# Performance work log

Hardware: AMD Instinct MI355X
Metric: run time of the kernel (lower is better)

Reference implementation:

```python
import jax, jax.numpy as jnp
import numpy as np
import math

N, D, H, KV, DH, E, F_, CH = 2048, 1024, 16, 4, 64, 8, 2048, 64
VOCAB = 32000
EPS = 1e-6
THETA = 10000.0
DT = 0.1
BASE_SCALE = 10.0


def rmsnorm(x, w):
    var = jnp.mean(jnp.square(x), axis=-1, keepdims=True)
    return x * jax.lax.rsqrt(var + EPS) * w


def rope_tables(positions):
    inv_freq = THETA ** (-jnp.arange(0, DH, 2, dtype=jnp.float32) / DH)  # [DH/2]
    ang = positions.astype(jnp.float32)[:, None] * inv_freq              # [N, DH/2]
    return jnp.cos(ang), jnp.sin(ang)


def apply_rotary(x, cos, sin):
    # x: [N, heads, DH]; NeoX half-split rotation
    x1, x2 = jnp.split(x, 2, axis=-1)
    c, s = cos[:, None, :], sin[:, None, :]
    return jnp.concatenate([x1 * c - x2 * s, x2 * c + x1 * s], axis=-1)


def setup_inputs() -> dict:
    key = jax.random.key(0)
    ks = jax.random.split(key, 20)
    nrm = lambda k, shp, std: (jax.random.normal(k, shp) * std).astype(jnp.float32)
    inp = {
        'hidden': jax.random.normal(ks[0], (N, D), jnp.float32),
        'positions': jnp.arange(N, dtype=jnp.int32),
        'velocity': jax.random.normal(ks[1], (N, D), jnp.float32) * 0.1,
        'token_ids': jax.random.randint(ks[2], (N,), 0, VOCAB),
        'mu_prev': jax.random.normal(ks[3], (N, D), jnp.float32) * 0.1,
        'ln1_w': jnp.ones((D,), jnp.float32),
        'ln2_w': jnp.ones((D,), jnp.float32),
        'wq': nrm(ks[4], (D, H * DH), 0.02),
        'wk': nrm(ks[5], (D, KV * DH), 0.02),
        'wv': nrm(ks[6], (D, KV * DH), 0.02),
        'wo': nrm(ks[7], (H * DH, D), 0.02),
        'w_mu_q': nrm(ks[8], (D, H * DH), 0.01),
        'w_mu_k': nrm(ks[9], (D, KV * DH), 0.01),
        'w_mu_v': nrm(ks[10], (D, KV * DH), 0.01),
        'qnorm_w': jnp.ones((DH,), jnp.float32),
        'knorm_w': jnp.ones((DH,), jnp.float32),
        'dyn_mu': jnp.zeros((D,), jnp.float32),
        'dyn_mu_proj_w': nrm(ks[11], (D, D), 0.01),
        'ctrl_in_w': nrm(ks[12], (2 * D, CH), 0.02),
        'ctrl_in_b': jnp.zeros((CH,), jnp.float32),
        'ctrl_out_w': nrm(ks[13], (CH, 3 * D), 0.01),
        'ctrl_out_b': jnp.concatenate([jnp.full((D,), 2.2), jnp.full((D,), -2.2), jnp.zeros((D,))]).astype(jnp.float32),
        'mu_router_w': nrm(ks[14], (D, E), 0.01),
        'w_gate': nrm(ks[15], (E, D, F_), 0.02),
        'w_up': nrm(ks[16], (E, D, F_), 0.02),
        'w_down': nrm(ks[17], (E, F_, D), 0.02),
    }
    return inp


def reference(hidden, positions, velocity, token_ids, mu_prev,
              ln1_w, ln2_w, wq, wk, wv, wo, w_mu_q, w_mu_k, w_mu_v,
              qnorm_w, knorm_w, dyn_mu, dyn_mu_proj_w,
              ctrl_in_w, ctrl_in_b, ctrl_out_w, ctrl_out_b,
              mu_router_w, w_gate, w_up, w_down):
    residual = hidden
    h = rmsnorm(hidden, ln1_w)
    # --- mu-guided GQA attention ---
    q = (h @ wq + mu_prev @ w_mu_q).reshape(N, H, DH)
    k = (h @ wk + mu_prev @ w_mu_k).reshape(N, KV, DH)
    v = (h @ wv + mu_prev @ w_mu_v).reshape(N, KV, DH)
    q = rmsnorm(q, qnorm_w)
    k = rmsnorm(k, knorm_w)
    cos, sin = rope_tables(positions)
    q = apply_rotary(q, cos, sin)
    k = apply_rotary(k, cos, sin)
    groups = H // KV
    k = jnp.repeat(k, groups, axis=1)  # [N, H, DH]
    v = jnp.repeat(v, groups, axis=1)
    scale = 1.0 / math.sqrt(DH)
    scores = jnp.einsum('nhd,mhd->hnm', q, k) * scale
    attn = jax.nn.softmax(scores, axis=-1)
    o = jnp.einsum('hnm,mhd->nhd', attn, v).reshape(N, H * DH) @ wo
    # --- INL dynamics (PID) ---
    hv = jnp.concatenate([o, velocity], axis=-1)
    ctrl = jax.nn.silu(hv @ ctrl_in_w + ctrl_in_b)
    co = ctrl @ ctrl_out_w + ctrl_out_b
    alpha_raw, beta_raw, gate_raw = co[:, :D], co[:, D:2 * D], co[:, 2 * D:]
    alpha = jax.nn.sigmoid(alpha_raw)
    beta = jnp.minimum(jax.nn.softplus(beta_raw), 2.0)
    gate = jax.nn.sigmoid(gate_raw)
    mu_cur = dyn_mu + o @ dyn_mu_proj_w
    err = o - mu_cur
    v_next = jnp.clip(alpha * velocity - beta * err, -10.0, 10.0)
    h_next = o + DT * gate * v_next
    hidden = residual + h_next
    # --- mu-guided token-routed MoE MLP ---
    residual2 = hidden
    x = rmsnorm(hidden, ln2_w)
    base_ids = (token_ids % E).astype(jnp.int32)
    mu_logits = mu_cur @ mu_router_w                        # [N, E]
    combined = jax.nn.one_hot(base_ids, E) * BASE_SCALE + mu_logits
    expert_ids = jnp.argmax(combined, axis=-1)              # [N]
    g = jnp.einsum('nd,edf->enf', x, w_gate)                # [E, N, F]
    u = jnp.einsum('nd,edf->enf', x, w_up)
    mid = jax.nn.silu(g) * u
    y_all = jnp.einsum('enf,efd->end', mid, w_down)         # [E, N, D]
    sel = jax.nn.one_hot(expert_ids, E)                     # [N, E]
    y = jnp.einsum('ne,end->nd', sel, y_all)
    hidden = residual2 + y
    return (hidden, v_next, mu_cur)
```

## Files before the change

### kernel.cpp

```cpp
#include <hip/hip_runtime.h>
#include <hip/hip_bf16.h>
#include <math.h>

typedef __hip_bfloat16 bf16;
typedef __attribute__((ext_vector_type(8))) short short8;
typedef __attribute__((ext_vector_type(4))) short short4v;
typedef __attribute__((ext_vector_type(4))) float floatx4;

#define N_TOK 2048
#define DM    1024
#define NH    16
#define NKV   4
#define DH    64
#define NE    8
#define FF    2048
#define CH    64
#define QSCL  0.18033688011112042f

__device__ __forceinline__ float b2f(bf16 x) { return __bfloat162float(x); }
__device__ __forceinline__ bf16  f2b(float x) { return __float2bfloat16(x); }
__device__ __forceinline__ short f2s(float x) { bf16 t = __float2bfloat16(x); return *(short*)&t; }

#define MFMA16(a, b, c) __builtin_amdgcn_mfma_f32_16x16x32_bf16(a, b, c, 0, 0, 0)

#define GLL16(g, l) __builtin_amdgcn_global_load_lds( \
    (const __attribute__((address_space(1))) void*)(g), \
    (__attribute__((address_space(3))) void*)(l), 16, 0, 0)

__device__ __forceinline__ float blockReduceSum256(float v) {
    __shared__ float tmp[4];
    #pragma unroll
    for (int m = 1; m < 64; m <<= 1) v += __shfl_xor(v, m, 64);
    if ((threadIdx.x & 63) == 0) tmp[threadIdx.x >> 6] = v;
    __syncthreads();
    float r = tmp[0] + tmp[1] + tmp[2] + tmp[3];
    __syncthreads();
    return r;
}

struct TEnt {
    const float* src; bf16* dst;
    long sstride, dstride;
    int sN, ldk, tN, tilesPer, start;
};
struct TTab { TEnt t[13]; };

template <int TK>
__global__ __launch_bounds__(256) void k_transpose_all(TTab tab, int base,
                                                       int* counts, int* fill) {
    if (base == 0 && blockIdx.x == 0 && threadIdx.x < NE) {
        counts[threadIdx.x] = 0;
        fill[threadIdx.x] = 0;
    }
    int b = blockIdx.x + base;
    int wi = 0;
    #pragma unroll
    for (int i = 1; i < 13; i++) if (b >= tab.t[i].start) wi = i;
    const TEnt& w = tab.t[wi];
    int local = b - w.start;
    int e = local / w.tilesPer; local -= e * w.tilesPer;
    int kt = local / w.tN, nt = local - kt * w.tN;
    const float* s = w.src + (long)e * w.sstride + (long)(kt * TK) * w.sN + nt * 64;
    bf16* d = w.dst + (long)e * w.dstride + (long)(nt * 64) * w.ldk + kt * TK;

    __shared__ short t16[64 * TK];
    int tid = threadIdx.x;
    int c4 = (tid & 15) * 4;

    #pragma unroll
    for (int j = 0; j < (TK / 8 + 15) / 16; j++) {
        int kk8 = 8 * ((tid >> 4) + 16 * j);
        if (kk8 < TK) {
            float4 rr[8];
            #pragma unroll
            for (int t = 0; t < 8; t++)
                rr[t] = *(const float4*)(s + (long)(kk8 + t) * w.sN + c4);
            #pragma unroll
            for (int q = 0; q < 4; q++) {
                int n = c4 + q;
                int ks = kk8 ^ ((n & 7) << 3);
                short8 o;
                #pragma unroll
                for (int t = 0; t < 8; t++) o[t] = f2s(((const float*)&rr[t])[q]);
                *(short8*)&t16[n * TK + ks] = o;
            }
        }
    }
    __syncthreads();
    const int cpr = TK / 8;
    #pragma unroll
    for (int rnd = 0; rnd < TK / 32; rnd++) {
        int id = tid + rnd * 256;
        int n = id / cpr;
        int kc = (id % cpr) * 8;
        int ks = kc ^ ((n & 7) << 3);
        short8 o = *(const short8*)&t16[n * TK + ks];
        *(short8*)(d + (long)n * w.ldk + kc) = o;
    }
}

__global__ __launch_bounds__(256) void k_prep(
    const float* __restrict__ hidden, const float* __restrict__ ln1_w,
    const float* __restrict__ mu_prev, const float* __restrict__ velocity,
    bf16* __restrict__ catA, bf16* __restrict__ ctrlA)
{
    int n = blockIdx.x, tid = threadIdx.x;
    float ss = 0.f, vals[4];
    #pragma unroll
    for (int i = 0; i < 4; i++) {
        int c = tid + i * 256;
        vals[i] = hidden[(long)n * DM + c];
        ss += vals[i] * vals[i];
        catA[(long)n * 2048 + 1024 + c] = f2b(mu_prev[(long)n * DM + c]);
        ctrlA[(long)n * 2048 + 1024 + c] = f2b(velocity[(long)n * DM + c]);
    }
    float tot = blockReduceSum256(ss);
    float r = rsqrtf(tot / (float)DM + 1e-6f);
    #pragma unroll
    for (int i = 0; i < 4; i++) {
        int c = tid + i * 256;
        catA[(long)n * 2048 + c] = f2b(vals[i] * r * ln1_w[c]);
    }
}

#define GEMM_WRITE  1
#define GEMM_BIAS   2
#define GEMM_WRITEB 4

__global__ __launch_bounds__(256) void k_gemm(
    const bf16* __restrict__ A, int lda,
    const bf16* __restrict__ Bt, int ldb, long strideBe,
    float* __restrict__ C, int ldc,
    const float* __restrict__ bias,
    bf16* __restrict__ Cb, int ldcb,
    int K, int flags,
    int nsplit, long strideKc,
    const int* __restrict__ grp_cnt)
{
    __shared__ __align__(16) short As[128 * 32];
    __shared__ __align__(16) short Bs[128 * 32];
    int tid = threadIdx.x;
    int e = blockIdx.z, kc = 0;
    if (nsplit > 1) { e = blockIdx.z / nsplit; kc = blockIdx.z % nsplit; }
    int rowBase, rowsValid;
    const bf16* Bp = Bt;
    if (grp_cnt) {
        int r0 = 0;
        #pragma unroll
        for (int i = 0; i < NE; i++) r0 += (i < e) ? grp_cnt[i] : 0;
        int r1 = r0 + grp_cnt[e];
        int rt = blockIdx.y * 128;
        rowsValid = (r1 - r0) - rt;
        if (rowsValid <= 0) return;
        if (rowsValid > 128) rowsValid = 128;
        rowBase = r0 + rt;
        Bp = Bt + (long)e * strideBe;
    } else {
        rowBase = blockIdx.y * 128;
        rowsValid = 128;
    }
    int n0 = blockIdx.x * 128;
    int Kc = K / nsplit;
    int kbeg = kc * Kc, kend = kbeg + Kc;

    floatx4 acc[4][4];
    #pragma unroll
    for (int i = 0; i < 4; i++)
        #pragma unroll
        for (int j = 0; j < 4; j++) acc[i][j] = (floatx4){0.f, 0.f, 0.f, 0.f};

    int wave = tid >> 6, lane = tid & 63;
    int wm = (wave >> 1) * 64, wn = (wave & 1) * 64;
    int lrow = lane & 15, quad = lane >> 4;

    int c0 = wave * 2;
    int srow0 = c0 * 16 + (lane >> 2);
    int srow1 = (c0 + 1) * 16 + (lane >> 2);
    int skoff = (lane & 3) * 8;
    short* ldsA0 = As + c0 * 512;
    short* ldsA1 = As + (c0 + 1) * 512;
    short* ldsB0 = Bs + c0 * 512;
    short* ldsB1 = Bs + (c0 + 1) * 512;

    for (int k0 = kbeg; k0 < kend; k0 += 32) {
        if (srow0 < rowsValid) GLL16(A + (long)(rowBase + srow0) * lda + k0 + skoff, ldsA0);
        if (srow1 < rowsValid) GLL16(A + (long)(rowBase + srow1) * lda + k0 + skoff, ldsA1);
        GLL16(Bp + (long)(n0 + srow0) * ldb + k0 + skoff, ldsB0);
        GLL16(Bp + (long)(n0 + srow1) * ldb + k0 + skoff, ldsB1);
        __syncthreads();
        short8 af[4], bfr[4];
        #pragma unroll
        for (int mi = 0; mi < 4; mi++)
            af[mi] = *(const short8*)(&As[(wm + mi * 16 + lrow) * 32 + quad * 8]);
        #pragma unroll
        for (int ni = 0; ni < 4; ni++)
            bfr[ni] = *(const short8*)(&Bs[(wn + ni * 16 + lrow) * 32 + quad * 8]);
        #pragma unroll
        for (int mi = 0; mi < 4; mi++)
            #pragma unroll
            for (int ni = 0; ni < 4; ni++)
                acc[mi][ni] = MFMA16(af[mi], bfr[ni], acc[mi][ni]);
        __syncthreads();
    }

    #pragma unroll
    for (int mi = 0; mi < 4; mi++) {
        #pragma unroll
        for (int ni = 0; ni < 4; ni++) {
            #pragma unroll
            for (int r = 0; r < 4; r++) {
                int rl = wm + mi * 16 + quad * 4 + r;
                if (rl >= rowsValid) continue;
                int grow = rowBase + rl;
                int gcol = n0 + wn + ni * 16 + lrow;
                float v = acc[mi][ni][r];
                if (nsplit > 1) {
                    C[kc * strideKc + (long)grow * ldc + gcol] = v;
                    continue;
                }
                if (flags & GEMM_BIAS) v += bias[gcol];
                if (flags & GEMM_WRITE) C[(long)grow * ldc + gcol] = v;
                if (flags & GEMM_WRITEB) Cb[(long)grow * ldcb + gcol] = f2b(v);
            }
        }
    }
}

__global__ __launch_bounds__(256) void k_gemm_f32b(
    const bf16* __restrict__ A, int lda,
    const float* __restrict__ Bf0, const float* __restrict__ Bf1,
    int ldbn, long strideBfe, int nbf0,
    float* __restrict__ C, int ldc,
    bf16* __restrict__ Cb, int ldcb,
    int K, int flags,
    int nsplit, long strideKc,
    const int* __restrict__ grp_cnt)
{
    __shared__ __align__(16) short As[128 * 32];
    __shared__ __align__(16) float Braw[32 * 128];
    __shared__ __align__(16) short Bs2[128 * 40];
    int tid = threadIdx.x;
    int e = blockIdx.z, kc = 0;
    if (nsplit > 1) { e = blockIdx.z / nsplit; kc = blockIdx.z % nsplit; }
    int r0 = 0;
    #pragma unroll
    for (int i = 0; i < NE; i++) r0 += (i < e) ? grp_cnt[i] : 0;
    int r1 = r0 + grp_cnt[e];
    int rt = blockIdx.y * 128;
    int rowsValid = (r1 - r0) - rt;
    if (rowsValid <= 0) return;
    if (rowsValid > 128) rowsValid = 128;
    int rowBase = r0 + rt;

    int n0 = blockIdx.x * 128;
    const float* Bsrc;
    int nb;
    if (n0 < nbf0) { Bsrc = Bf0; nb = n0; }
    else           { Bsrc = Bf1; nb = n0 - nbf0; }
    Bsrc += (long)e * strideBfe;

    int Kc = K / nsplit;
    int kbeg = kc * Kc, kend = kbeg + Kc;

    floatx4 acc[4][4];
    #pragma unroll
    for (int i = 0; i < 4; i++)
        #pragma unroll
        for (int j = 0; j < 4; j++) acc[i][j] = (floatx4){0.f, 0.f, 0.f, 0.f};

    int wave = tid >> 6, lane = tid & 63;
    int wm = (wave >> 1) * 64, wn = (wave & 1) * 64;
    int lrow = lane & 15, quad = lane >> 4;

    int c0 = wave * 2;
    int srow0 = c0 * 16 + (lane >> 2);
    int srow1 = (c0 + 1) * 16 + (lane >> 2);
    int skoff = (lane & 3) * 8;
    short* ldsA0 = As + c0 * 512;
    short* ldsA1 = As + (c0 + 1) * 512;

    int kB = wave * 2 + (lane >> 5);
    int ncB = (lane & 31) * 4;

    for (int k0 = kbeg; k0 < kend; k0 += 32) {
        if (srow0 < rowsValid) GLL16(A + (long)(rowBase + srow0) * lda + k0 + skoff, ldsA0);
        if (srow1 < rowsValid) GLL16(A + (long)(rowBase + srow1) * lda + k0 + skoff, ldsA1);
        #pragma unroll
        for (int r = 0; r < 4; r++)
            GLL16(Bsrc + (long)(k0 + r * 8 + kB) * ldbn + nb + ncB,
                  Braw + r * 1024 + wave * 256);
        __syncthreads();

        #pragma unroll
        for (int r2 = 0; r2 < 4; r2++) {
            int id = r2 * 256 + tid;
            int n = id & 127, kb = id >> 7;
            float f0 = Braw[(kb * 4 + 0) * 128 + n];
            float f1 = Braw[(kb * 4 + 1) * 128 + n];
            float f2 = Braw[(kb * 4 + 2) * 128 + n];
            float f3 = Braw[(kb * 4 + 3) * 128 + n];
            short4v o;
            o[0] = f2s(f0); o[1] = f2s(f1); o[2] = f2s(f2); o[3] = f2s(f3);
            *(short4v*)&Bs2[n * 40 + kb * 4] = o;
        }
        short8 af[4];
        #pragma unroll
        for (int mi = 0; mi < 4; mi++)
            af[mi] = *(const short8*)(&As[(wm + mi * 16 + lrow) * 32 + quad * 8]);
        __syncthreads();

        short8 bfr[4];
        #pragma unroll
        for (int ni = 0; ni < 4; ni++)
            bfr[ni] = *(const short8*)(&Bs2[(wn + ni * 16 + lrow) * 40 + quad * 8]);
        #pragma unroll
        for (int mi = 0; mi < 4; mi++)
            #pragma unroll
            for (int ni = 0; ni < 4; ni++)
                acc[mi][ni] = MFMA16(af[mi], bfr[ni], acc[mi][ni]);
    }
    __syncthreads();

    #pragma unroll
    for (int mi = 0; mi < 4; mi++) {
        #pragma unroll
        for (int ni = 0; ni < 4; ni++) {
            #pragma unroll
            for (int r = 0; r < 4; r++) {
                int rl = wm + mi * 16 + quad * 4 + r;
                if (rl >= rowsValid) continue;
                int grow = rowBase + rl;
                int gcol = n0 + wn + ni * 16 + lrow;
                float v = acc[mi][ni][r];
                if (nsplit > 1) {
                    C[kc * strideKc + (long)grow * ldc + gcol] = v;
                } else if (flags & GEMM_WRITEB) {
                    Cb[(long)grow * ldcb + gcol] = f2b(v);
                }
            }
        }
    }
}

__global__ __launch_bounds__(256) void k_red_wo(const float* __restrict__ p,
                                                float* __restrict__ o_f,
                                                bf16* __restrict__ ctrlA) {
    int n = blockIdx.x, tid = threadIdx.x;
    #pragma unroll
    for (int i = 0; i < 4; i++) {
        int c = tid + i * 256;
        float v = p[(long)n * DM + c] + p[(long)N_TOK * DM + (long)n * DM + c];
        o_f[(long)n * DM + c] = v;
        ctrlA[(long)n * 2048 + c] = f2b(v);
    }
}

__global__ __launch_bounds__(256) void k_red_down(const float* __restrict__ p,
                                                  const int* __restrict__ perm,
                                                  float* __restrict__ out0) {
    int r = blockIdx.x, tid = threadIdx.x;
    int tok = perm[r];
    #pragma unroll
    for (int i = 0; i < 4; i++) {
        int c = tid + i * 256;
        long idx = (long)r * DM + c;
        float v = p[idx] + p[(long)N_TOK * DM + idx] +
                  p[(long)2 * N_TOK * DM + idx] + p[(long)3 * N_TOK * DM + idx];
        out0[(long)tok * DM + c] += v;
    }
}

__global__ __launch_bounds__(256) void k_ctrl_gemm(
    const bf16* __restrict__ A,
    const bf16* __restrict__ Bt,
    float* __restrict__ part)
{
    __shared__ __align__(16) short As[128 * 32];
    __shared__ __align__(16) short Bs[64 * 32];
    int tid = threadIdx.x;
    int rowBase = blockIdx.x * 128;
    int kbeg = blockIdx.y * 256;
    int wave = tid >> 6, lane = tid & 63;
    int wm = wave * 32, lrow = lane & 15, quad = lane >> 4;
    int srow = lane >> 2, skoff = (lane & 3) * 8;

    floatx4 acc[2][4];
    #pragma unroll
    for (int i = 0; i < 2; i++)
        #pragma unroll
        for (int j = 0; j < 4; j++) acc[i][j] = (floatx4){0.f, 0.f, 0.f, 0.f};

    short* ldsA0 = As + (wave * 2) * 512;
    short* ldsA1 = As + (wave * 2 + 1) * 512;
    short* ldsB  = Bs + wave * 512;

    for (int k0 = kbeg; k0 < kbeg + 256; k0 += 32) {
        GLL16(A + (long)(rowBase + wave * 32 + srow) * 2048 + k0 + skoff, ldsA0);
        GLL16(A + (long)(rowBase + wave * 32 + 16 + srow) * 2048 + k0 + skoff, ldsA1);
        GLL16(Bt + (long)(wave * 16 + srow) * 2048 + k0 + skoff, ldsB);
        __syncthreads();
        short8 af[2], bfr[4];
        af[0] = *(const short8*)(&As[(wm + lrow) * 32 + quad * 8]);
        af[1] = *(const short8*)(&As[(wm + 16 + lrow) * 32 + quad * 8]);
        #pragma unroll
        for (int ni = 0; ni < 4; ni++)
            bfr[ni] = *(const short8*)(&Bs[(ni * 16 + lrow) * 32 + quad * 8]);
        #pragma unroll
        for (int mi = 0; mi < 2; mi++)
            #pragma unroll
            for (int ni = 0; ni < 4; ni++)
                acc[mi][ni] = MFMA16(af[mi], bfr[ni], acc[mi][ni]);
        __syncthreads();
    }
    #pragma unroll
    for (int mi = 0; mi < 2; mi++)
        #pragma unroll
        for (int ni = 0; ni < 4; ni++)
            #pragma unroll
            for (int r = 0; r < 4; r++) {
                int grow = rowBase + wm + mi * 16 + quad * 4 + r;
                part[((long)blockIdx.y * N_TOK + grow) * 64 + ni * 16 + lrow] = acc[mi][ni][r];
            }
}

__global__ __launch_bounds__(256) void k_silu_ctrl(const float* __restrict__ part,
                                                   const float* __restrict__ b,
                                                   bf16* __restrict__ out) {
    int i4 = (blockIdx.x * 256 + threadIdx.x) * 4;
    float4 a = *(const float4*)(b + (i4 & 63));
    #pragma unroll
    for (int kc = 0; kc < 8; kc++) {
        float4 p = *(const float4*)(part + (long)kc * (N_TOK * 64) + i4);
        a.x += p.x; a.y += p.y; a.z += p.z; a.w += p.w;
    }
    short4v o;
    o[0] = f2s(a.x / (1.f + __expf(-a.x)));
    o[1] = f2s(a.y / (1.f + __expf(-a.y)));
    o[2] = f2s(a.z / (1.f + __expf(-a.z)));
    o[3] = f2s(a.w / (1.f + __expf(-a.w)));
    *(short4v*)(out + i4) = o;
}

__global__ __launch_bounds__(256) void k_qkv_post(
    const float* __restrict__ qkvp, const int* __restrict__ positions,
    const float* __restrict__ qnw, const float* __restrict__ knw,
    bf16* __restrict__ q, bf16* __restrict__ k, bf16* __restrict__ v)
{
    int n = blockIdx.x;
    int wave = threadIdx.x >> 6, lane = threadIdx.x & 63;
    float pos = (float)positions[n];
    int i = lane & 31;
    float invf = exp2f(-(float)(2 * i) * (13.287712379549449f / 64.f));
    float ang = pos * invf;
    float c = cosf(ang), s = sinf(ang);

    #pragma unroll
    for (int si = 0; si < 6; si++) {
        int slot = wave + si * 4;
        long base = (long)n * 1536 +
                    (slot < 16 ? slot * 64
                               : (slot < 20 ? 1024 + (slot - 16) * 64
                                            : 1280 + (slot - 20) * 64));
        float val = qkvp[base + lane] + qkvp[(long)N_TOK * 1536 + base + lane];
        if (slot < 20) {
            float ss = val * val;
            #pragma unroll
            for (int m = 1; m < 64; m <<= 1) ss += __shfl_xor(ss, m, 64);
            float r = rsqrtf(ss / 64.f + 1e-6f);
            float wn = (slot < 16 ? qnw[lane] : knw[lane]);
            float xn = val * r * wn;
            float partner = __shfl_xor(xn, 32, 64);
            float out = (lane < 32) ? (xn * c - partner * s) : (xn * c + partner * s);
            if (slot < 16) q[((long)n * NH + slot) * 64 + lane] = f2b(out * QSCL);
            else           k[((long)n * NKV + (slot - 16)) * 64 + lane] = f2b(out);
        } else {
            v[((long)n * NKV + (slot - 20)) * 64 + lane] = f2b(val);
        }
    }
}

__global__ __launch_bounds__(256) void k_vt(const bf16* __restrict__ v,
                                            bf16* __restrict__ vt) {
    __shared__ short tile[64][65];
    int kv = blockIdx.z, n0 = blockIdx.x * 64;
    int tid = threadIdx.x;
    int c = tid & 63, r4 = tid >> 6;
    const short* vs = (const short*)v;
    #pragma unroll
    for (int i = 0; i < 16; i++) {
        int r = i * 4 + r4;
        tile[r][c] = vs[(long)(n0 + r) * 256 + kv * 64 + c];
    }
    __syncthreads();
    #pragma unroll
    for (int i = 0; i < 16; i++) {
        int d = i * 4 + r4;
        ((short*)vt)[(long)(kv * 64 + d) * 2048 + n0 + c] = tile[c][d];
    }
}

__device__ __forceinline__ int lds_idx(int row, int col_sh) {
    int byteoff = col_sh * 2;
    byteoff ^= (row & 7) << 4;
    return row * 64 + (byteoff >> 1);
}

__global__ __launch_bounds__(256) void k_attn(
    const bf16* __restrict__ q, const bf16* __restrict__ k,
    const bf16* __restrict__ vt,
    float* __restrict__ opart, float2* __restrict__ ml)
{
    const int h = blockIdx.y;
    const int qbase = blockIdx.x * 64;
    const int z = blockIdx.z;
    const int kvh = h >> 2;
    __shared__ __align__(16) short Ks[64 * 64];
    __shared__ __align__(16) short Vt[64 * 64];
    __shared__ __align__(16) short Ps[64 * 64];
    int tid = threadIdx.x, wave = tid >> 6, lane = tid & 63;
    int lrow = lane & 15, quad = lane >> 4;

    const bf16* qp = q + ((long)(qbase + wave * 16 + lrow) * NH + h) * 64;
    short8 aq0 = *(const short8*)(qp + quad * 8);
    short8 aq1 = *(const short8*)(qp + 32 + quad * 8);

    short8 bones;
    #pragma unroll
    for (int j = 0; j < 8; j++) bones[j] = (short)0x3F80;

    const int lin0 = tid, lin1 = tid + 256;
    const int sr0 = lin0 >> 3, sc0 = (lin0 & 7) * 8;
    const int sr1 = lin1 >> 3, sc1 = (lin1 & 7) * 8;
    const int wi0 = lds_idx(sr0, sc0), wi1 = lds_idx(sr1, sc1);

    const int kt0 = z * (N_TOK / 4);
    const bf16* kg0 = k + ((long)(kt0 + sr0) * NKV + kvh) * 64 + sc0;
    const bf16* kg1 = k + ((long)(kt0 + sr1) * NKV + kvh) * 64 + sc1;
    const bf16* vg0 = vt + (long)(kvh * 64 + sr0) * 2048 + kt0 + sc0;
    const bf16* vg1 = vt + (long)(kvh * 64 + sr1) * 2048 + kt0 + sc1;

    *(short8*)&Ks[wi0] = *(const short8*)kg0;
    *(short8*)&Ks[wi1] = *(const short8*)kg1;
    *(short8*)&Vt[wi0] = *(const short8*)vg0;
    *(short8*)&Vt[wi1] = *(const short8*)vg1;

    float m_i[4];
    floatx4 lacc = (floatx4){0.f, 0.f, 0.f, 0.f};
    floatx4 oacc[4];
    #pragma unroll
    for (int r = 0; r < 4; r++) m_i[r] = -1e30f;
    #pragma unroll
    for (int di = 0; di < 4; di++) oacc[di] = (floatx4){0.f, 0.f, 0.f, 0.f};
    __syncthreads();

    const int NT = (N_TOK / 4) / 64;
    for (int t = 0; t < NT; t++) {
        bool pf = (t + 1 < NT);
        short8 nk0, nk1, nv0, nv1;
        if (pf) {
            long ko = (long)(t + 1) * (64 * NKV * 64);
            int  vo = (t + 1) * 64;
            nk0 = *(const short8*)(kg0 + ko);
            nk1 = *(const short8*)(kg1 + ko);
            nv0 = *(const short8*)(vg0 + vo);
            nv1 = *(const short8*)(vg1 + vo);
        }

        floatx4 sv[4];
        __builtin_amdgcn_s_setprio(1);
        #pragma unroll
        for (int kn = 0; kn < 4; kn++) {
            short8 b0 = *(const short8*)&Ks[lds_idx(kn * 16 + lrow, quad * 8)];
            short8 b1 = *(const short8*)&Ks[lds_idx(kn * 16 + lrow, 32 + quad * 8)];
            floatx4 tt = (floatx4){0.f, 0.f, 0.f, 0.f};
            tt = MFMA16(aq0, b0, tt);
            tt = MFMA16(aq1, b1, tt);
            sv[kn] = tt;
        }
        __builtin_amdgcn_s_setprio(0);

        float mx[4];
        #pragma unroll
        for (int r = 0; r < 4; r++) {
            float m0 = fmaxf(fmaxf(sv[0][r], sv[1][r]), fmaxf(sv[2][r], sv[3][r]));
            #pragma unroll
            for (int msk = 1; msk < 16; msk <<= 1) m0 = fmaxf(m0, __shfl_xor(m0, msk, 64));
            mx[r] = m0;
        }
        int ok = (mx[0] <= m_i[0] + 8.f) & (mx[1] <= m_i[1] + 8.f) &
                 (mx[2] <= m_i[2] + 8.f) & (mx[3] <= m_i[3] + 8.f);
        if (!__all(ok)) {
            #pragma unroll
            for (int r = 0; r < 4; r++) {
                float mn = fmaxf(m_i[r], mx[r]);
                float al = exp2f(m_i[r] - mn);
                m_i[r] = mn;
                lacc[r] *= al;
                #pragma unroll
                for (int di = 0; di < 4; di++) oacc[di][r] *= al;
            }
        }
        #pragma unroll
        for (int kn = 0; kn < 4; kn++)
            #pragma unroll
            for (int r = 0; r < 4; r++)
                sv[kn][r] = exp2f(sv[kn][r] - m_i[r]);

        #pragma unroll
        for (int kn = 0; kn < 4; kn++)
            #pragma unroll
            for (int r = 0; r < 4; r++)
                Ps[lds_idx(wave * 16 + quad * 4 + r, kn * 16 + lrow)] = f2s(sv[kn][r]);
        __syncthreads();

        short8 ap0 = *(const short8*)&Ps[lds_idx(wave * 16 + lrow, quad * 8)];
        short8 ap1 = *(const short8*)&Ps[lds_idx(wave * 16 + lrow, 32 + quad * 8)];
        __builtin_amdgcn_s_setprio(1);
        lacc = MFMA16(ap0, bones, lacc);
        lacc = MFMA16(ap1, bones, lacc);
        #pragma unroll
        for (int di = 0; di < 4; di++) {
            short8 bv0 = *(const short8*)&Vt[lds_idx(di * 16 + lrow, quad * 8)];
            short8 bv1 = *(const short8*)&Vt[lds_idx(di * 16 + lrow, 32 + quad * 8)];
            oacc[di] = MFMA16(ap0, bv0, oacc[di]);
            oacc[di] = MFMA16(ap1, bv1, oacc[di]);
        }
        __builtin_amdgcn_s_setprio(0);
        __syncthreads();

        if (pf) {
            *(short8*)&Ks[wi0] = nk0;
            *(short8*)&Ks[wi1] = nk1;
            *(short8*)&Vt[wi0] = nv0;
            *(short8*)&Vt[wi1] = nv1;
            __syncthreads();
        }
    }

    #pragma unroll
    for (int di = 0; di < 4; di++)
        #pragma unroll
        for (int r = 0; r < 4; r++) {
            int n = qbase + wave * 16 + quad * 4 + r;
            opart[((long)z * N_TOK + n) * DM + h * 64 + di * 16 + lrow] = oacc[di][r];
        }
    if (lrow == 0) {
        #pragma unroll
        for (int r = 0; r < 4; r++) {
            int n = qbase + wave * 16 + quad * 4 + r;
            ml[(long)(z * NH + h) * N_TOK + n] = make_float2(m_i[r], lacc[r]);
        }
    }
}

__global__ __launch_bounds__(256) void k_attn_merge(
    const float* __restrict__ opart, const float2* __restrict__ ml,
    bf16* __restrict__ attn_out)
{
    int n = blockIdx.x, tid = threadIdx.x;
    __shared__ float2 sml[4][NH];
    if (tid < 64) {
        int zz = tid >> 4, hh = tid & 15;
        sml[zz][hh] = ml[(long)(zz * NH + hh) * N_TOK + n];
    }
    __syncthreads();
    #pragma unroll
    for (int i = 0; i < 4; i++) {
        int c = tid + i * 256;
        int h = c >> 6;
        float M = fmaxf(fmaxf(sml[0][h].x, sml[1][h].x),
                        fmaxf(sml[2][h].x, sml[3][h].x));
        float num = 0.f, den = 0.f;
        #pragma unroll
        for (int zz = 0; zz < 4; zz++) {
            float w = exp2f(sml[zz][h].x - M);
            num += w * opart[((long)zz * N_TOK + n) * DM + c];
            den += w * sml[zz][h].y;
        }
        attn_out[(long)n * DM + c] = f2b(num / den);
    }
}

__global__ __launch_bounds__(256) void k_ode(
    const float* __restrict__ co, const float* __restrict__ o_f,
    const float* __restrict__ velocity, const float* __restrict__ mup,
    const float* __restrict__ dyn_mu, const float* __restrict__ hidden_in,
    const float* __restrict__ mu_router_w, const int* __restrict__ token_ids,
    const float* __restrict__ ln2_w,
    float* __restrict__ out0, float* __restrict__ out_vnext,
    float* __restrict__ out_mu, bf16* __restrict__ x_bf,
    int* __restrict__ expert_id, int* __restrict__ counts)
{
    int n = blockIdx.x, tid = threadIdx.x;
    __shared__ float mu_s[DM];
    __shared__ float red2[32][8];

    #pragma unroll
    for (int i = 0; i < 4; i++) {
        int c = tid + i * 256;
        mu_s[c] = mup[(long)n * DM + c] + mup[(long)N_TOK * DM + (long)n * DM + c]
                + dyn_mu[c];
    }
    __syncthreads();

    {
        int e = tid & 7, kc = tid >> 3;
        float a = 0.f;
        #pragma unroll
        for (int kk = 0; kk < 32; kk++) {
            int k = kc * 32 + kk;
            a += mu_s[k] * mu_router_w[k * NE + e];
        }
        red2[kc][e] = a;
    }
    __syncthreads();
    if (tid == 0) {
        int bid = token_ids[n] & (NE - 1);
        float best = -1e30f; int bi = 0;
        for (int e = 0; e < NE; e++) {
            float lg = (e == bid ? 10.f : 0.f);
            for (int j = 0; j < 32; j++) lg += red2[j][e];
            if (lg > best) { best = lg; bi = e; }
        }
        expert_id[n] = bi;
        atomicAdd(&counts[bi], 1);
    }

    float ssq = 0.f;
    float h1v[4];
    #pragma unroll
    for (int i = 0; i < 4; i++) {
        int c = tid + i * 256;
        float coa = co[(long)n * 3072 + c];
        float cob = co[(long)n * 3072 + DM + c];
        float cog = co[(long)n * 3072 + 2 * DM + c];
        float alpha = 1.f / (1.f + __expf(-coa));
        float sp = (cob > 20.f) ? cob : log1pf(__expf(cob));
        float beta = fminf(sp, 2.0f);
        float gate = 1.f / (1.f + __expf(-cog));
        float ov = o_f[(long)n * DM + c];
        float vv = velocity[(long)n * DM + c];
        float err = ov - mu_s[c];
        float vn = fminf(fmaxf(alpha * vv - beta * err, -10.f), 10.f);
        float hn = ov + 0.1f * gate * vn;
        float h1 = hidden_in[(long)n * DM + c] + hn;
        h1v[i] = h1;
        ssq += h1 * h1;
        out_vnext[(long)n * DM + c] = vn;
        out_mu[(long)n * DM + c] = mu_s[c];
        out0[(long)n * DM + c] = h1;
    }
    float tot = blockReduceSum256(ssq);
    float rstd = rsqrtf(tot / (float)DM + 1e-6f);
    #pragma unroll
    for (int i = 0; i < 4; i++) {
        int c = tid + i * 256;
        x_bf[(long)n * DM + c] = f2b(h1v[i] * rstd * ln2_w[c]);
    }
}

__global__ __launch_bounds__(256) void k_scatter_gather(
    const int* __restrict__ expert_id, const int* __restrict__ counts,
    int* __restrict__ fill, int* __restrict__ perm,
    const bf16* __restrict__ x, bf16* __restrict__ xg)
{
    int n = blockIdx.x * 4 + (threadIdx.x >> 6);
    int lane = threadIdx.x & 63;
    int e = expert_id[n];
    int p = 0;
    if (lane == 0) {
        int off = 0;
        #pragma unroll
        for (int i = 0; i < NE; i++) off += (i < e) ? counts[i] : 0;
        p = off + atomicAdd(&fill[e], 1);
        perm[p] = n;
    }
    p = __shfl(p, 0, 64);
    const int4* s = (const int4*)(x + (long)n * DM);
    int4* d = (int4*)(xg + (long)p * DM);
    d[lane] = s[lane];
    d[lane + 64] = s[lane + 64];
}

__global__ __launch_bounds__(256) void k_silumul(const bf16* __restrict__ gu,
                                                 bf16* __restrict__ mid) {
    long i = ((long)blockIdx.x * 256 + threadIdx.x) * 8;
    long r = i >> 11, c = i & 2047;
    short8 g8 = *(const short8*)(gu + r * 4096 + c);
    short8 u8 = *(const short8*)(gu + r * 4096 + 2048 + c);
    short8 o;
    #pragma unroll
    for (int j = 0; j < 8; j++) {
        short gs = g8[j], us = u8[j];
        float g = b2f(*(bf16*)&gs);
        float u = b2f(*(bf16*)&us);
        o[j] = f2s(g / (1.f + __expf(-g)) * u);
    }
    *(short8*)(mid + i) = o;
}

extern "C" void kernel_launch(void* const* d_in, const int* in_sizes, int n_in,
                              void* d_out, int out_size, void* d_ws, size_t ws_size,
                              hipStream_t stream) {
    (void)in_sizes; (void)n_in; (void)out_size; (void)ws_size;
    const float* hidden     = (const float*)d_in[0];
    const int*   positions  = (const int*)d_in[1];
    const float* velocity   = (const float*)d_in[2];
    const int*   token_ids  = (const int*)d_in[3];
    const float* mu_prev    = (const float*)d_in[4];
    const float* ln1_w      = (const float*)d_in[5];
    const float* ln2_w      = (const float*)d_in[6];
    const float* wq         = (const float*)d_in[7];
    const float* wk         = (const float*)d_in[8];
    const float* wv         = (const float*)d_in[9];
    const float* wo         = (const float*)d_in[10];
    const float* w_mu_q     = (const float*)d_in[11];
    const float* w_mu_k     = (const float*)d_in[12];
    const float* w_mu_v     = (const float*)d_in[13];
    const float* qnorm_w    = (const float*)d_in[14];
    const float* knorm_w    = (const float*)d_in[15];
    const float* dyn_mu     = (const float*)d_in[16];
    const float* dyn_proj   = (const float*)d_in[17];
    const float* ctrl_in_w  = (const float*)d_in[18];
    const float* ctrl_in_b  = (const float*)d_in[19];
    const float* ctrl_out_w = (const float*)d_in[20];
    const float* ctrl_out_b = (const float*)d_in[21];
    const float* mu_router  = (const float*)d_in[22];
    const float* w_gate     = (const float*)d_in[23];
    const float* w_up       = (const float*)d_in[24];
    const float* w_down     = (const float*)d_in[25];

    float* out0 = (float*)d_out;
    float* out1 = out0 + (long)N_TOK * DM;
    float* out2 = out1 + (long)N_TOK * DM;

    char* p = (char*)d_ws;
    auto alloc = [&](size_t bytes) -> void* {
        void* r = (void*)p;
        p += (bytes + 255) & ~(size_t)255;
        return r;
    };
    bf16* WqkvT   = (bf16*)alloc((long)1536 * 2048 * 2);
    bf16* woT     = (bf16*)alloc((long)1024 * 1024 * 2);
    bf16* dynT    = (bf16*)alloc((long)1024 * 1024 * 2);
    bf16* ctrlinT = (bf16*)alloc((long)64 * 2048 * 2);
    bf16* ctrloutT= (bf16*)alloc((long)3072 * 64 * 2);
    bf16*  catA   = (bf16*)alloc((long)N_TOK * 2048 * 2);
    bf16*  ctrlA  = (bf16*)alloc((long)N_TOK * 2048 * 2);
    float* xbuf   = (float*)alloc((long)N_TOK * 1536 * 4);
    bf16*  q_bf   = (bf16*)alloc((long)N_TOK * NH * DH * 2);
    bf16*  k_bf   = (bf16*)alloc((long)N_TOK * NKV * DH * 2);
    bf16*  v_bf   = (bf16*)alloc((long)N_TOK * NKV * DH * 2);
    bf16*  vt_bf  = (bf16*)alloc((long)NKV * DH * N_TOK * 2);
    float* o_f    = (float*)alloc((long)N_TOK * DM * 4);
    float* coGu   = (float*)alloc((long)N_TOK * 3072 * 4);
    float* splitb = (float*)alloc((long)4 * N_TOK * DM * 4);
    bf16*  ctrlbf = (bf16*)alloc((long)N_TOK * CH * 2);
    int*   expert_id = (int*)alloc(N_TOK * 4);
    int*   perm      = (int*)alloc(N_TOK * 4);
    int*   counts    = (int*)alloc(64 * 4);
    int*   fill      = (int*)alloc(64 * 4);

    bf16*  attn_bf = catA;
    bf16*  x_bf    = (bf16*)xbuf;
    bf16*  xg_bf   = (bf16*)xbuf + (long)N_TOK * DM;
    float* cpart   = (float*)((bf16*)xbuf + (long)2 * N_TOK * DM);
    float* opart   = splitb;
    float2* ml     = (float2*)coGu;
    float* co_f    = coGu;
    bf16*  gu_bf   = (bf16*)coGu;
    bf16*  mid_bf  = (bf16*)o_f;

    dim3 blk(256);

    TTab tt{};
    int st = 0;
    auto ent = [&](int i, const float* s, bf16* d, long ss, long ds,
                   int sN, int ldk, int tN, int tK, int nE) {
        tt.t[i].src = s; tt.t[i].dst = d;
        tt.t[i].sstride = ss; tt.t[i].dstride = ds;
        tt.t[i].sN = sN; tt.t[i].ldk = ldk;
        tt.t[i].tN = tN; tt.t[i].tilesPer = tN * tK;
        tt.t[i].start = st;
        st += tN * tK * nE;
    };
    ent(0,  wq,         WqkvT,                          0, 0, 1024, 2048, 16, 4, 1);
    ent(1,  wk,         WqkvT + (long)1024 * 2048,      0, 0, 256,  2048,  4, 4, 1);
    ent(2,  wv,         WqkvT + (long)1280 * 2048,      0, 0, 256,  2048,  4, 4, 1);
    ent(3,  w_mu_q,     WqkvT + 1024,                   0, 0, 1024, 2048, 16, 4, 1);
    ent(4,  w_mu_k,     WqkvT + (long)1024 * 2048 + 1024, 0, 0, 256, 2048, 4, 4, 1);
    ent(5,  w_mu_v,     WqkvT + (long)1280 * 2048 + 1024, 0, 0, 256, 2048, 4, 4, 1);
    ent(6,  wo,         woT,                            0, 0, 1024, 1024, 16, 4, 1);
    ent(7,  dyn_proj,   dynT,                           0, 0, 1024, 1024, 16, 4, 1);
    ent(8,  ctrl_in_w,  ctrlinT,                        0, 0, 64,   2048,  1, 8, 1);
    int stMain = st;
    ent(9,  ctrl_out_w, ctrloutT,                       0, 0, 3072, 64,   48, 1, 1);
    tt.t[10].start = 0x7fffffff;
    tt.t[11].start = 0x7fffffff;
    tt.t[12].start = 0x7fffffff;
    k_transpose_all<256><<<stMain, blk, 0, stream>>>(tt, 0, counts, fill);
    k_transpose_all<64><<<st - stMain, blk, 0, stream>>>(tt, stMain, counts, fill);

    k_prep<<<N_TOK, blk, 0, stream>>>(hidden, ln1_w, mu_prev, velocity, catA, ctrlA);

    k_gemm<<<dim3(12,16,2), blk, 0, stream>>>(catA, 2048, WqkvT, 2048, 0,
        splitb, 1536, nullptr, nullptr, 0, 2048, 0, 2, (long)N_TOK * 1536,
        nullptr);

    k_qkv_post<<<N_TOK, blk, 0, stream>>>(splitb, positions, qnorm_w, knorm_w, q_bf, k_bf, v_bf);
    k_vt<<<dim3(32,1,NKV), blk, 0, stream>>>(v_bf, vt_bf);
    k_attn<<<dim3(32,16,4), blk, 0, stream>>>(q_bf, k_bf, vt_bf, opart, ml);
    k_attn_merge<<<N_TOK, blk, 0, stream>>>(opart, ml, attn_bf);

    k_gemm<<<dim3(8,16,2), blk, 0, stream>>>(attn_bf, 1024, woT, 1024, 0,
        splitb, 1024, nullptr, nullptr, 0, 1024, 0, 2, (long)N_TOK * DM,
        nullptr);
    k_red_wo<<<N_TOK, blk, 0, stream>>>(splitb, o_f, ctrlA);

    k_gemm<<<dim3(8,16,2), blk, 0, stream>>>(ctrlA, 2048, dynT, 1024, 0,
        splitb, 1024, nullptr, nullptr, 0, 1024, 0, 2, (long)N_TOK * DM,
        nullptr);

    k_ctrl_gemm<<<dim3(16,8,1), blk, 0, stream>>>(ctrlA, ctrlinT, cpart);
    k_silu_ctrl<<<(N_TOK * CH) / 1024, blk, 0, stream>>>(cpart, ctrl_in_b, ctrlbf);
    k_gemm<<<dim3(24,16,1), blk, 0, stream>>>(ctrlbf, 64, ctrloutT, 64, 0,
        co_f, 3072, ctrl_out_b, nullptr, 0, 64, GEMM_WRITE | GEMM_BIAS, 1, 0,
        nullptr);

    k_ode<<<N_TOK, blk, 0, stream>>>(co_f, o_f, velocity, splitb, dyn_mu, hidden,
        mu_router, token_ids, ln2_w, out0, out1, out2, x_bf, expert_id, counts);

    k_scatter_gather<<<N_TOK / 4, blk, 0, stream>>>(expert_id, counts, fill, perm,
        x_bf, xg_bf);

    k_gemm_f32b<<<dim3(32,16,NE), blk, 0, stream>>>(xg_bf, 1024,
        w_gate, w_up, 2048, (long)1024 * 2048, 2048,
        nullptr, 0, gu_bf, 4096, 1024, GEMM_WRITEB, 1, 0, counts);
    k_silumul<<<(N_TOK * FF) / (256 * 8), blk, 0, stream>>>(gu_bf, mid_bf);
    k_gemm_f32b<<<dim3(8,16,NE*4), blk, 0, stream>>>(mid_bf, 2048,
        w_down, w_down, 1024, (long)2048 * 1024, 1 << 30,
        splitb, 1024, nullptr, 0, 2048, 0, 4, (long)N_TOK * DM, counts);
    k_red_down<<<N_TOK, blk, 0, stream>>>(splitb, perm, out0);
}
```

Measured before the change: 578.1 us.

## Register-prefetch and double-buffer LDS in grouped fp32-weight GEMM

Replaces the direct global-to-LDS loads and staging fp32 buffer with register prefetch of the next A/B tile. The fp32 B values are converted to bf16 in registers and written straight into a double-buffered LDS tile, which removes the Braw staging pass and one barrier per K step. The intent is to overlap global loads with MFMA work and cut LDS traffic. In exchange it uses more registers, which may lower occupancy, and invalid A rows are clamped to the last valid row rather than skipped.

Result: no change. 579.5 us (+0.2%).

```diff
diff --git a/kernel.cpp b/kernel.cpp
--- a/kernel.cpp
+++ b/kernel.cpp
@@ -236,9 +236,8 @@
     int nsplit, long strideKc,
     const int* __restrict__ grp_cnt)
 {
-    __shared__ __align__(16) short As[128 * 32];
-    __shared__ __align__(16) float Braw[32 * 128];
-    __shared__ __align__(16) short Bs2[128 * 40];
+    __shared__ __align__(16) short As[2][128 * 32];
+    __shared__ __align__(16) short Bs2[2][128 * 40];
     int tid = threadIdx.x;
     int e = blockIdx.z, kc = 0;
     if (nsplit > 1) { e = blockIdx.z / nsplit; kc = blockIdx.z % nsplit; }
@@ -272,54 +271,54 @@
     int wm = (wave >> 1) * 64, wn = (wave & 1) * 64;
     int lrow = lane & 15, quad = lane >> 4;
 
-    int c0 = wave * 2;
-    int srow0 = c0 * 16 + (lane >> 2);
-    int srow1 = (c0 + 1) * 16 + (lane >> 2);
-    int skoff = (lane & 3) * 8;
-    short* ldsA0 = As + c0 * 512;
-    short* ldsA1 = As + (c0 + 1) * 512;
-
-    int kB = wave * 2 + (lane >> 5);
-    int ncB = (lane & 31) * 4;
+    int arow = tid >> 1, ak = (tid & 1) * 16;
+    int arowc = (arow < rowsValid) ? arow : (rowsValid - 1);
+    const bf16* Aptr = A + (long)(rowBase + arowc) * lda + ak;
+    int n4 = (tid & 31) * 4;
+    int kp4 = (tid >> 5) * 4;
+    const float* Bptr = Bsrc + (long)kp4 * ldbn + nb + n4;
+
+    int4 a0, a1;
+    float4 br[4];
+    auto loadAB = [&](int k0) {
+        a0 = *(const int4*)(Aptr + k0);
+        a1 = *(const int4*)(Aptr + k0 + 8);
+        const float* bp = Bptr + (long)k0 * ldbn;
+        #pragma unroll
+        for (int r = 0; r < 4; r++)
+            br[r] = *(const float4*)(bp + (long)r * ldbn);
+    };
+    loadAB(kbeg);
 
     for (int k0 = kbeg; k0 < kend; k0 += 32) {
-        if (srow0 < rowsValid) GLL16(A + (long)(rowBase + srow0) * lda + k0 + skoff, ldsA0);
-        if (srow1 < rowsValid) GLL16(A + (long)(rowBase + srow1) * lda + k0 + skoff, ldsA1);
-        #pragma unroll
-        for (int r = 0; r < 4; r++)
-            GLL16(Bsrc + (long)(k0 + r * 8 + kB) * ldbn + nb + ncB,
-                  Braw + r * 1024 + wave * 256);
+        int cur = ((k0 - kbeg) >> 5) & 1;
+        *(int4*)&As[cur][arow * 32 + ak] = a0;
+        *(int4*)&As[cur][arow * 32 + ak + 8] = a1;
+        #pragma unroll
+        for (int q = 0; q < 4; q++) {
+            short4v o;
+            o[0] = f2s(((const float*)&br[0])[q]);
+            o[1] = f2s(((const float*)&br[1])[q]);
+            o[2] = f2s(((const float*)&br[2])[q]);
+            o[3] = f2s(((const float*)&br[3])[q]);
+            *(short4v*)&Bs2[cur][(n4 + q) * 40 + kp4] = o;
+        }
+        if (k0 + 32 < kend) loadAB(k0 + 32);
         __syncthreads();
 
-        #pragma unroll
-        for (int r2 = 0; r2 < 4; r2++) {
-            int id = r2 * 256 + tid;
-            int n = id & 127, kb = id >> 7;
-            float f0 = Braw[(kb * 4 + 0) * 128 + n];
-            float f1 = Braw[(kb * 4 + 1) * 128 + n];
-            float f2 = Braw[(kb * 4 + 2) * 128 + n];
-            float f3 = Braw[(kb * 4 + 3) * 128 + n];
-            short4v o;
-            o[0] = f2s(f0); o[1] = f2s(f1); o[2] = f2s(f2); o[3] = f2s(f3);
-            *(short4v*)&Bs2[n * 40 + kb * 4] = o;
-        }
-        short8 af[4];
+        short8 af[4], bfr[4];
         #pragma unroll
         for (int mi = 0; mi < 4; mi++)
-            af[mi] = *(const short8*)(&As[(wm + mi * 16 + lrow) * 32 + quad * 8]);
-        __syncthreads();
-
-        short8 bfr[4];
+            af[mi] = *(const short8*)(&As[cur][(wm + mi * 16 + lrow) * 32 + quad * 8]);
         #pragma unroll
         for (int ni = 0; ni < 4; ni++)
-            bfr[ni] = *(const short8*)(&Bs2[(wn + ni * 16 + lrow) * 40 + quad * 8]);
+            bfr[ni] = *(const short8*)(&Bs2[cur][(wn + ni * 16 + lrow) * 40 + quad * 8]);
         #pragma unroll
         for (int mi = 0; mi < 4; mi++)
             #pragma unroll
             for (int ni = 0; ni < 4; ni++)
                 acc[mi][ni] = MFMA16(af[mi], bfr[ni], acc[mi][ni]);
     }
-    __syncthreads();
 
     #pragma unroll
     for (int mi = 0; mi < 4; mi++) {
```
